# Kernel optimization log

Hardware: AMD Instinct MI355X
Metric: run time of the kernel (lower is better)

The kernel has to match this reference:

```python
import jax, jax.numpy as jnp
import numpy as np

T, B, U = 256, 4, 64
E_ENC, E_DEC, J, V = 1024, 640, 640, 4096
LN_EPS = 1e-5


def layer_norm(x, gamma, beta):
    mu = jnp.mean(x, axis=-1, keepdims=True)
    var = jnp.mean(jnp.square(x - mu), axis=-1, keepdims=True)
    return (x - mu) * jax.lax.rsqrt(var + LN_EPS) * gamma + beta


def setup_inputs() -> dict:
    key = jax.random.key(0)
    ks = jax.random.split(key, 8)
    inp = {
        "encoder_out": jax.random.normal(ks[0], (T, B, E_ENC), dtype=jnp.float32),
        "decoder_out": jax.random.normal(ks[1], (U, B, E_DEC), dtype=jnp.float32),
        # proj_encoder
        "W_enc": jax.random.normal(ks[2], (J, E_ENC), dtype=jnp.float32) * (E_ENC ** -0.5),
        "b_enc": jnp.zeros((J,), dtype=jnp.float32),
        "g_enc": jnp.ones((J,), dtype=jnp.float32),
        "be_enc": jnp.zeros((J,), dtype=jnp.float32),
        # proj_decoder
        "W_dec": jax.random.normal(ks[3], (J, E_DEC), dtype=jnp.float32) * (E_DEC ** -0.5),
        "b_dec": jnp.zeros((J,), dtype=jnp.float32),
        "g_dec": jnp.ones((J,), dtype=jnp.float32),
        "be_dec": jnp.zeros((J,), dtype=jnp.float32),
        # fc_out (init.normal_ with std = joint_dim**-0.5)
        "W_out": jax.random.normal(ks[4], (V, J), dtype=jnp.float32) * (J ** -0.5),
        "b_out": jnp.zeros((V,), dtype=jnp.float32),
    }
    return inp


def reference(encoder_out, decoder_out, W_enc, b_enc, g_enc, be_enc,
              W_dec, b_dec, g_dec, be_dec, W_out, b_out):
    # encoder_out: [T, B, E_enc] -> project+LN -> transpose -> [B, T, J]
    enc = layer_norm(jnp.einsum('tbe,je->tbj', encoder_out, W_enc) + b_enc,
                     g_enc, be_enc).transpose(1, 0, 2)
    # decoder_out: [U, B, E_dec] -> [B, U, J]
    dec = layer_norm(jnp.einsum('ube,je->ubj', decoder_out, W_dec) + b_dec,
                     g_dec, be_dec).transpose(1, 0, 2)
    # broadcast outer-sum over T x U, then ReLU: [B, T, U, J]
    joint = jax.nn.relu(enc[:, :, None, :] + dec[:, None, :, :])
    # vocab projection: [B, T, U, V]
    return jnp.einsum('btuj,vj->btuv', joint, W_out) + b_out
```

## Files before the change

### kernel.cpp

```cpp
#include <hip/hip_runtime.h>
#include <stdint.h>

#define T_    256
#define B_    4
#define U_    64
#define EENC  1024
#define EDEC  640
#define J_    640
#define V_    4096

typedef unsigned short u16;
typedef unsigned int   u32;
typedef __bf16 bf16x8 __attribute__((ext_vector_type(8)));
typedef short  s16x8  __attribute__((ext_vector_type(8)));
typedef float  f32x4  __attribute__((ext_vector_type(4)));

__device__ __forceinline__ u16 f2bf(float f) {
    u32 u = __builtin_bit_cast(u32, f);
    u = (u + 0x7FFFu + ((u >> 16) & 1u)) >> 16;
    return (u16)u;
}
__device__ __forceinline__ float bf2f(u16 b) {
    return __builtin_bit_cast(float, (u32)b << 16);
}

__global__ __launch_bounds__(256) void cvt_bf16(const float* __restrict__ src,
                                                u16* __restrict__ dst, int n4) {
    int i = blockIdx.x * 256 + threadIdx.x;
    if (i < n4) {
        float4 v = reinterpret_cast<const float4*>(src)[i];
        ushort4 o;
        o.x = f2bf(v.x); o.y = f2bf(v.y); o.z = f2bf(v.z); o.w = f2bf(v.w);
        reinterpret_cast<ushort4*>(dst)[i] = o;
    }
}

__global__ __launch_bounds__(256) void ln_kernel(const float* __restrict__ proj,
                                                 const float* __restrict__ bias,
                                                 const float* __restrict__ gamma,
                                                 const float* __restrict__ beta,
                                                 u16* __restrict__ out,
                                                 int BDIM, int OUTER) {
    int pr = blockIdx.x;
    int b = pr % BDIM, outer = pr / BDIM;
    const float* row = proj + (size_t)pr * J_;
    int tid = threadIdx.x;

    float x0 = row[tid] + bias[tid];
    float x1 = row[tid + 256] + bias[tid + 256];
    float x2 = 0.f;
    bool has3 = (tid < J_ - 512);
    if (has3) x2 = row[tid + 512] + bias[tid + 512];

    float s1 = x0 + x1 + x2;
    float s2 = x0 * x0 + x1 * x1 + x2 * x2;
    for (int off = 32; off; off >>= 1) {
        s1 += __shfl_down(s1, off, 64);
        s2 += __shfl_down(s2, off, 64);
    }
    __shared__ float ws1[4], ws2[4];
    int w = tid >> 6, lane = tid & 63;
    if (lane == 0) { ws1[w] = s1; ws2[w] = s2; }
    __syncthreads();
    float S1 = ws1[0] + ws1[1] + ws1[2] + ws1[3];
    float S2 = ws2[0] + ws2[1] + ws2[2] + ws2[3];
    float mu = S1 * (1.f / J_);
    float var = S2 * (1.f / J_) - mu * mu;
    float inv = 1.0f / sqrtf(var + 1e-5f);

    size_t orow = ((size_t)b * OUTER + outer) * J_;
    out[orow + tid]       = f2bf((x0 - mu) * inv * gamma[tid]       + beta[tid]);
    out[orow + tid + 256] = f2bf((x1 - mu) * inv * gamma[tid + 256] + beta[tid + 256]);
    if (has3)
        out[orow + tid + 512] = f2bf((x2 - mu) * inv * gamma[tid + 512] + beta[tid + 512]);
}

__global__ __launch_bounds__(256) void joint_mat(const u16* __restrict__ encln,
                                                 const u16* __restrict__ decln,
                                                 u16* __restrict__ joint) {
    int g = blockIdx.x * 256 + threadIdx.x;
    int row = g / (J_ / 8);
    int jc = g - row * (J_ / 8);
    int b = row >> 14;
    int t = (row >> 6) & (T_ - 1);
    int u = row & (U_ - 1);
    s16x8 e = *reinterpret_cast<const s16x8*>(encln + ((size_t)(b * T_ + t)) * J_ + jc * 8);
    s16x8 d = *reinterpret_cast<const s16x8*>(decln + ((size_t)(b * U_ + u)) * J_ + jc * 8);
    s16x8 o;
#pragma unroll
    for (int k = 0; k < 8; ++k) {
        float v = bf2f((u16)e[k]) + bf2f((u16)d[k]);
        o[k] = (short)f2bf(fmaxf(v, 0.f));
    }
    *reinterpret_cast<s16x8*>(joint + (size_t)row * J_ + jc * 8) = o;
}

__global__ __launch_bounds__(256) void gemm_bt(const u16* __restrict__ A,
                                               const u16* __restrict__ Bt,
                                               float* __restrict__ C,
                                               const float* __restrict__ bias,
                                               int K, int ldc) {
    __shared__ u16 As[128 * 64];
    __shared__ u16 Bs[128 * 64];
    const int tid = threadIdx.x;
    const int w = tid >> 6, lane = tid & 63;
    const int wr = w >> 1, wc = w & 1;
    const size_t m0 = (size_t)blockIdx.y * 128;
    const size_t n0 = (size_t)blockIdx.x * 128;

    f32x4 acc[4][4] = {};

    const int l3 = lane >> 3;
    const int c8 = (lane & 7) * 8;
    const int nkt = K >> 6;

    for (int kt = 0; kt < nkt; ++kt) {
        if (kt) __syncthreads();
        const int k0 = kt << 6;
#pragma unroll
        for (int i = 0; i < 4; ++i) {
            const int c = w * 4 + i;
            const int r = c * 8 + l3;
            const u16* ga = A  + (m0 + r) * (size_t)K + k0 + c8;
            const u16* gb = Bt + (n0 + r) * (size_t)K + k0 + c8;
            __builtin_amdgcn_global_load_lds(
                (const __attribute__((address_space(1))) void*)ga,
                (__attribute__((address_space(3))) void*)(As + c * 512), 16, 0, 0);
            __builtin_amdgcn_global_load_lds(
                (const __attribute__((address_space(1))) void*)gb,
                (__attribute__((address_space(3))) void*)(Bs + c * 512), 16, 0, 0);
        }
        __syncthreads();

#pragma unroll
        for (int kk = 0; kk < 2; ++kk) {
            bf16x8 af[4], bfr[4];
#pragma unroll
            for (int i = 0; i < 4; ++i) {
                int ra = wr * 64 + i * 16 + (lane & 15);
                af[i] = *reinterpret_cast<const bf16x8*>(As + ra * 64 + kk * 32 + (lane >> 4) * 8);
                int rb = wc * 64 + i * 16 + (lane & 15);
                bfr[i] = *reinterpret_cast<const bf16x8*>(Bs + rb * 64 + kk * 32 + (lane >> 4) * 8);
            }
#pragma unroll
            for (int i = 0; i < 4; ++i)
#pragma unroll
                for (int j = 0; j < 4; ++j)
                    acc[i][j] = __builtin_amdgcn_mfma_f32_16x16x32_bf16(af[i], bfr[j], acc[i][j], 0, 0, 0);
        }
    }

    const int r4 = (lane >> 4) * 4;
    const int cl = lane & 15;
#pragma unroll
    for (int i = 0; i < 4; ++i) {
#pragma unroll
        for (int j = 0; j < 4; ++j) {
            size_t grow = m0 + wr * 64 + i * 16 + r4;
            size_t gcol = n0 + wc * 64 + j * 16 + cl;
            float bv = bias ? bias[gcol] : 0.f;
#pragma unroll
            for (int r = 0; r < 4; ++r)
                C[(grow + r) * (size_t)ldc + gcol] = acc[i][j][r] + bv;
        }
    }
}

#define BK   64
#define BIGK 640
#define BIGN 4096
#define NT_  (BIGK / BK)

__global__ __launch_bounds__(512, 2) void gemm_big(const u16* __restrict__ A,
                                                   const u16* __restrict__ Bt,
                                                   float* __restrict__ C,
                                                   const float* __restrict__ bias) {
    __shared__ u16 lds[2][2][256 * BK];

    const int tid = threadIdx.x;
    const int w = tid >> 6, lane = tid & 63;
    const int wr = w >> 2, wc = w & 3;
    const int fr = lane & 15, fq = lane >> 4;

    const int lin = blockIdx.x;
    const int xcd = lin & 7;
    const int idx = lin >> 3;
    const size_t m0 = (size_t)(idx >> 1) * 256;
    const size_t n0 = (size_t)(xcd * 2 + (idx & 1)) * 256;

    const int srow = lane >> 3;
    const int scol = ((lane & 7) * 16) ^ (srow << 4);
    const u16* agbase = A  + (m0 + w * 8 + srow) * (size_t)BIGK + (scol >> 1);
    const u16* bgbase = Bt + (n0 + w * 8 + srow) * (size_t)BIGK + (scol >> 1);
    const int ldst = (w * 8) * BK;

    f32x4 acc[8][4] = {};

#define STAGE_A(buf, c, k0)                                                        \
    __builtin_amdgcn_global_load_lds(                                              \
        (const __attribute__((address_space(1))) void*)(agbase + (size_t)(c) * 64 * BIGK + (k0)), \
        (__attribute__((address_space(3))) void*)(&lds[buf][0][(c) * 64 * BK + ldst]), 16, 0, 0)
#define STAGE_B(buf, c, k0)                                                        \
    __builtin_amdgcn_global_load_lds(                                              \
        (const __attribute__((address_space(1))) void*)(bgbase + (size_t)(c) * 64 * BIGK + (k0)), \
        (__attribute__((address_space(3))) void*)(&lds[buf][1][(c) * 64 * BK + ldst]), 16, 0, 0)

#define RD_A(buf, mh, mi, kk)                                                      \
    (*reinterpret_cast<const bf16x8*>(&lds[buf][0][                                \
        (wr * 128 + (mh) * 64 + (mi) * 16 + fr) * BK +                             \
        ((((kk) * 64 + fq * 16) ^ ((fr & 7) << 4)) >> 1)]))
#define RD_B(buf, ni, kk)                                                          \
    (*reinterpret_cast<const bf16x8*>(&lds[buf][1][                                \
        (wc * 64 + (ni) * 16 + fr) * BK +                                          \
        ((((kk) * 64 + fq * 16) ^ ((fr & 7) << 4)) >> 1)]))

#define WAIT2 asm volatile("s_waitcnt vmcnt(2)" ::: "memory")
#define WAIT0 asm volatile("s_waitcnt vmcnt(0)" ::: "memory")
#define LGKM0 asm volatile("s_waitcnt lgkmcnt(0)" ::: "memory")

    STAGE_B(0, 0, 0); STAGE_B(0, 1, 0); STAGE_B(0, 2, 0); STAGE_B(0, 3, 0);
    STAGE_A(0, 0, 0); STAGE_A(0, 2, 0); STAGE_A(0, 1, 0); STAGE_A(0, 3, 0);
    WAIT2;
    __builtin_amdgcn_s_barrier();

    for (int t = 0; t < NT_; ++t) {
        const int cur = t & 1, nxt = cur ^ 1;
        const int kn = (t + 1) << 6;
        const bool pf = (t + 1 < NT_);
        bf16x8 af[4], b0[4], b1[4];

#pragma unroll
        for (int i = 0; i < 4; ++i) af[i] = RD_A(cur, 0, i, 0);
#pragma unroll
        for (int j = 0; j < 4; ++j) b0[j] = RD_B(cur, j, 0);
        if (pf) { STAGE_B(nxt, 0, kn); STAGE_B(nxt, 1, kn); }
        __builtin_amdgcn_s_barrier();
        LGKM0;
        __builtin_amdgcn_s_setprio(1);
#pragma unroll
        for (int i = 0; i < 4; ++i)
#pragma unroll
            for (int j = 0; j < 4; ++j)
                acc[i][j] = __builtin_amdgcn_mfma_f32_16x16x32_bf16(af[i], b0[j], acc[i][j], 0, 0, 0);
        __builtin_amdgcn_s_setprio(0);
        if (pf) WAIT2; else WAIT0;
        __builtin_amdgcn_s_barrier();

#pragma unroll
        for (int i = 0; i < 4; ++i) af[i] = RD_A(cur, 1, i, 0);
        if (pf) { STAGE_B(nxt, 2, kn); STAGE_B(nxt, 3, kn); }
        __builtin_amdgcn_s_barrier();
        LGKM0;
        __builtin_amdgcn_s_setprio(1);
#pragma unroll
        for (int i = 0; i < 4; ++i)
#pragma unroll
            for (int j = 0; j < 4; ++j)
                acc[4 + i][j] = __builtin_amdgcn_mfma_f32_16x16x32_bf16(af[i], b0[j], acc[4 + i][j], 0, 0, 0);
        __builtin_amdgcn_s_setprio(0);
        __builtin_amdgcn_s_barrier();

#pragma unroll
        for (int i = 0; i < 4; ++i) af[i] = RD_A(cur, 0, i, 1);
#pragma unroll
        for (int j = 0; j < 4; ++j) b1[j] = RD_B(cur, j, 1);
        if (pf) { STAGE_A(nxt, 0, kn); STAGE_A(nxt, 2, kn); }
        __builtin_amdgcn_s_barrier();
        LGKM0;
        __builtin_amdgcn_s_setprio(1);
#pragma unroll
        for (int i = 0; i < 4; ++i)
#pragma unroll
            for (int j = 0; j < 4; ++j)
                acc[i][j] = __builtin_amdgcn_mfma_f32_16x16x32_bf16(af[i], b1[j], acc[i][j], 0, 0, 0);
        __builtin_amdgcn_s_setprio(0);
        __builtin_amdgcn_s_barrier();

#pragma unroll
        for (int i = 0; i < 4; ++i) af[i] = RD_A(cur, 1, i, 1);
        if (pf) { STAGE_A(nxt, 1, kn); STAGE_A(nxt, 3, kn); }
        __builtin_amdgcn_s_barrier();
        LGKM0;
        __builtin_amdgcn_s_setprio(1);
#pragma unroll
        for (int i = 0; i < 4; ++i)
#pragma unroll
            for (int j = 0; j < 4; ++j)
                acc[4 + i][j] = __builtin_amdgcn_mfma_f32_16x16x32_bf16(af[i], b1[j], acc[4 + i][j], 0, 0, 0);
        __builtin_amdgcn_s_setprio(0);
        if (pf) WAIT2;
        __builtin_amdgcn_s_barrier();
    }

#undef STAGE_A
#undef STAGE_B
#undef RD_A
#undef RD_B
#undef WAIT2
#undef WAIT0
#undef LGKM0

    const size_t crow0 = m0 + wr * 128 + fq * 4;
    const size_t ccol0 = n0 + wc * 64 + fr;
#pragma unroll
    for (int ni = 0; ni < 4; ++ni) {
        const size_t col = ccol0 + ni * 16;
        const float bv = bias[col];
#pragma unroll
        for (int mi = 0; mi < 8; ++mi) {
            const size_t rbase = crow0 + mi * 16;
#pragma unroll
            for (int r = 0; r < 4; ++r)
                __builtin_nontemporal_store(acc[mi][ni][r] + bv,
                                            &C[(rbase + r) * (size_t)BIGN + col]);
        }
    }
}

static const size_t O_JOINT = 0;
static const size_t O_WOUT  = 83886080;
static const size_t O_ENCLN = 89128960;
static const size_t O_DECLN = 90439680;
static const size_t O_ENCIN = 90767360;
static const size_t O_DECIN = 92864512;
static const size_t O_WENC  = 93192192;
static const size_t O_WDEC  = 94502912;
static const size_t O_EPROJ = 95322112;
static const size_t O_DPROJ = 97943552;
static const size_t WS_NEEDED = 98598912;

extern "C" void kernel_launch(void* const* d_in, const int* in_sizes, int n_in,
                              void* d_out, int out_size, void* d_ws, size_t ws_size,
                              hipStream_t stream) {
    const float* enc   = (const float*)d_in[0];
    const float* dec   = (const float*)d_in[1];
    const float* Wenc  = (const float*)d_in[2];
    const float* benc  = (const float*)d_in[3];
    const float* genc  = (const float*)d_in[4];
    const float* beenc = (const float*)d_in[5];
    const float* Wdec  = (const float*)d_in[6];
    const float* bdec  = (const float*)d_in[7];
    const float* gdec  = (const float*)d_in[8];
    const float* bedec = (const float*)d_in[9];
    const float* Wout  = (const float*)d_in[10];
    const float* bout  = (const float*)d_in[11];
    float* out = (float*)d_out;

    if (ws_size < WS_NEEDED) return;

    char* ws = (char*)d_ws;
    u16* joint  = (u16*)(ws + O_JOINT);
    u16* wout_b = (u16*)(ws + O_WOUT);
    u16* encln  = (u16*)(ws + O_ENCLN);
    u16* decln  = (u16*)(ws + O_DECLN);
    u16* encin  = (u16*)(ws + O_ENCIN);
    u16* decin  = (u16*)(ws + O_DECIN);
    u16* wenc_b = (u16*)(ws + O_WENC);
    u16* wdec_b = (u16*)(ws + O_WDEC);
    float* eproj = (float*)(ws + O_EPROJ);
    float* dproj = (float*)(ws + O_DPROJ);

    cvt_bf16<<<1024, 256, 0, stream>>>(enc,  encin,  (T_ * B_ * EENC) / 4);
    cvt_bf16<<<160,  256, 0, stream>>>(dec,  decin,  (U_ * B_ * EDEC) / 4);
    cvt_bf16<<<640,  256, 0, stream>>>(Wenc, wenc_b, (J_ * EENC) / 4);
    cvt_bf16<<<400,  256, 0, stream>>>(Wdec, wdec_b, (J_ * EDEC) / 4);
    cvt_bf16<<<2560, 256, 0, stream>>>(Wout, wout_b, (V_ * J_) / 4);

    gemm_bt<<<dim3(J_ / 128, (T_ * B_) / 128), 256, 0, stream>>>(encin, wenc_b, eproj, nullptr, EENC, J_);
    gemm_bt<<<dim3(J_ / 128, (U_ * B_) / 128), 256, 0, stream>>>(decin, wdec_b, dproj, nullptr, EDEC, J_);

    ln_kernel<<<T_ * B_, 256, 0, stream>>>(eproj, benc, genc, beenc, encln, B_, T_);
    ln_kernel<<<U_ * B_, 256, 0, stream>>>(dproj, bdec, gdec, bedec, decln, B_, U_);

    joint_mat<<<(B_ * T_ * U_ * (J_ / 8)) / 256, 256, 0, stream>>>(encln, decln, joint);

    gemm_big<<<(B_ * T_ * U_ / 256) * (V_ / 256), 512, 0, stream>>>(joint, wout_b, out, bout);
}
```

Measured before the change: 533.6 us.

## Fuse joint add+ReLU into big GEMM A-tile loading, drop joint buffer

Removes the separate joint_mat kernel and its large bf16 joint intermediate. The big GEMM now builds its A tile on the fly: it loads encoder and decoder LN rows into registers, adds them, applies ReLU, packs to bf16 and writes the result into swizzled LDS. This saves an extra write and read of the joint tensor in HBM. In exchange, A staging goes through registers instead of async global_load_lds, and the pipeline waits change to full vmcnt(0), which may expose more load latency.

Result: slower. 617.6 us (+15.7%).

```diff
diff --git a/kernel.cpp b/kernel.cpp
--- a/kernel.cpp
+++ b/kernel.cpp
@@ -22,6 +22,24 @@
 }
 __device__ __forceinline__ float bf2f(u16 b) {
     return __builtin_bit_cast(float, (u32)b << 16);
+}
+
+__device__ __forceinline__ u32 joint2(u32 e, u32 d) {
+    float elo = __builtin_bit_cast(float, e << 16);
+    float ehi = __builtin_bit_cast(float, e & 0xFFFF0000u);
+    float dlo = __builtin_bit_cast(float, d << 16);
+    float dhi = __builtin_bit_cast(float, d & 0xFFFF0000u);
+    float slo = fmaxf(elo + dlo, 0.f);
+    float shi = fmaxf(ehi + dhi, 0.f);
+    u32 r;
+    asm("v_cvt_pk_bf16_f32 %0, %1, %2" : "=v"(r) : "v"(slo), "v"(shi));
+    return r;
+}
+__device__ __forceinline__ uint4 joint4(uint4 e, uint4 d) {
+    uint4 j;
+    j.x = joint2(e.x, d.x); j.y = joint2(e.y, d.y);
+    j.z = joint2(e.z, d.z); j.w = joint2(e.w, d.w);
+    return j;
 }
 
 __global__ __launch_bounds__(256) void cvt_bf16(const float* __restrict__ src,
@@ -73,26 +91,6 @@
     out[orow + tid + 256] = f2bf((x1 - mu) * inv * gamma[tid + 256] + beta[tid + 256]);
     if (has3)
         out[orow + tid + 512] = f2bf((x2 - mu) * inv * gamma[tid + 512] + beta[tid + 512]);
-}
-
-__global__ __launch_bounds__(256) void joint_mat(const u16* __restrict__ encln,
-                                                 const u16* __restrict__ decln,
-                                                 u16* __restrict__ joint) {
-    int g = blockIdx.x * 256 + threadIdx.x;
-    int row = g / (J_ / 8);
-    int jc = g - row * (J_ / 8);
-    int b = row >> 14;
-    int t = (row >> 6) & (T_ - 1);
-    int u = row & (U_ - 1);
-    s16x8 e = *reinterpret_cast<const s16x8*>(encln + ((size_t)(b * T_ + t)) * J_ + jc * 8);
-    s16x8 d = *reinterpret_cast<const s16x8*>(decln + ((size_t)(b * U_ + u)) * J_ + jc * 8);
-    s16x8 o;
-#pragma unroll
-    for (int k = 0; k < 8; ++k) {
-        float v = bf2f((u16)e[k]) + bf2f((u16)d[k]);
-        o[k] = (short)f2bf(fmaxf(v, 0.f));
-    }
-    *reinterpret_cast<s16x8*>(joint + (size_t)row * J_ + jc * 8) = o;
 }
 
 __global__ __launch_bounds__(256) void gemm_bt(const u16* __restrict__ A,
@@ -171,7 +169,8 @@
 #define BIGN 4096
 #define NT_  (BIGK / BK)
 
-__global__ __launch_bounds__(512, 2) void gemm_big(const u16* __restrict__ A,
+__global__ __launch_bounds__(512, 2) void gemm_big(const u16* __restrict__ encln,
+                                                   const u16* __restrict__ decln,
                                                    const u16* __restrict__ Bt,
                                                    float* __restrict__ C,
                                                    const float* __restrict__ bias) {
@@ -185,25 +184,50 @@
     const int lin = blockIdx.x;
     const int xcd = lin & 7;
     const int idx = lin >> 3;
-    const size_t m0 = (size_t)(idx >> 1) * 256;
+    const int mt  = idx >> 1;
+    const size_t m0 = (size_t)mt * 256;
     const size_t n0 = (size_t)(xcd * 2 + (idx & 1)) * 256;
+
+    const int b  = mt >> 6;
+    const int t0 = (mt & 63) << 2;
+
+    const int r  = tid >> 1;
+    const int h  = tid & 1;
+    const int tq = r >> 6;
+    const int uu = r & 63;
+    const int xr = (r & 7) << 4;
+    const u16* encrow = encln + (size_t)(b * T_ + t0 + tq) * J_ + 32 * h;
+    const u16* decrow = decln + (size_t)(b * U_ + uu) * J_ + 32 * h;
+    const int aw0 = r * BK + ((( 0 + 64 * h) ^ xr) >> 1);
+    const int aw1 = r * BK + (((16 + 64 * h) ^ xr) >> 1);
+    const int aw2 = r * BK + (((32 + 64 * h) ^ xr) >> 1);
+    const int aw3 = r * BK + (((48 + 64 * h) ^ xr) >> 1);
 
     const int srow = lane >> 3;
     const int scol = ((lane & 7) * 16) ^ (srow << 4);
-    const u16* agbase = A  + (m0 + w * 8 + srow) * (size_t)BIGK + (scol >> 1);
     const u16* bgbase = Bt + (n0 + w * 8 + srow) * (size_t)BIGK + (scol >> 1);
     const int ldst = (w * 8) * BK;
 
     f32x4 acc[8][4] = {};
 
-#define STAGE_A(buf, c, k0)                                                        \
-    __builtin_amdgcn_global_load_lds(                                              \
-        (const __attribute__((address_space(1))) void*)(agbase + (size_t)(c) * 64 * BIGK + (k0)), \
-        (__attribute__((address_space(3))) void*)(&lds[buf][0][(c) * 64 * BK + ldst]), 16, 0, 0)
 #define STAGE_B(buf, c, k0)                                                        \
     __builtin_amdgcn_global_load_lds(                                              \
         (const __attribute__((address_space(1))) void*)(bgbase + (size_t)(c) * 64 * BIGK + (k0)), \
         (__attribute__((address_space(3))) void*)(&lds[buf][1][(c) * 64 * BK + ldst]), 16, 0, 0)
+
+#define A_LOAD(kt)                                                                 \
+    { const u16* ep = encrow + (size_t)(kt) * BK;                                  \
+      const u16* dp = decrow + (size_t)(kt) * BK;                                  \
+      ev0 = *(const uint4*)(ep);      dv0 = *(const uint4*)(dp);                   \
+      ev1 = *(const uint4*)(ep + 8);  dv1 = *(const uint4*)(dp + 8);               \
+      ev2 = *(const uint4*)(ep + 16); dv2 = *(const uint4*)(dp + 16);              \
+      ev3 = *(const uint4*)(ep + 24); dv3 = *(const uint4*)(dp + 24); }
+
+#define A_WRITE(buf)                                                               \
+    { *(uint4*)(&lds[buf][0][aw0]) = joint4(ev0, dv0);                             \
+      *(uint4*)(&lds[buf][0][aw1]) = joint4(ev1, dv1);                             \
+      *(uint4*)(&lds[buf][0][aw2]) = joint4(ev2, dv2);                             \
+      *(uint4*)(&lds[buf][0][aw3]) = joint4(ev3, dv3); }
 
 #define RD_A(buf, mh, mi, kk)                                                      \
     (*reinterpret_cast<const bf16x8*>(&lds[buf][0][                                \
@@ -214,20 +238,25 @@
         (wc * 64 + (ni) * 16 + fr) * BK +                                          \
         ((((kk) * 64 + fq * 16) ^ ((fr & 7) << 4)) >> 1)]))
 
-#define WAIT2 asm volatile("s_waitcnt vmcnt(2)" ::: "memory")
-#define WAIT0 asm volatile("s_waitcnt vmcnt(0)" ::: "memory")
+#define VM0   asm volatile("s_waitcnt vmcnt(0)" ::: "memory")
 #define LGKM0 asm volatile("s_waitcnt lgkmcnt(0)" ::: "memory")
 
-    STAGE_B(0, 0, 0); STAGE_B(0, 1, 0); STAGE_B(0, 2, 0); STAGE_B(0, 3, 0);
-    STAGE_A(0, 0, 0); STAGE_A(0, 2, 0); STAGE_A(0, 1, 0); STAGE_A(0, 3, 0);
-    WAIT2;
-    __builtin_amdgcn_s_barrier();
+    {
+        uint4 ev0, ev1, ev2, ev3, dv0, dv1, dv2, dv3;
+        STAGE_B(0, 0, 0); STAGE_B(0, 1, 0); STAGE_B(0, 2, 0); STAGE_B(0, 3, 0);
+        A_LOAD(0);
+        A_WRITE(0);
+        VM0;
+        LGKM0;
+        __builtin_amdgcn_s_barrier();
+    }
 
     for (int t = 0; t < NT_; ++t) {
         const int cur = t & 1, nxt = cur ^ 1;
         const int kn = (t + 1) << 6;
         const bool pf = (t + 1 < NT_);
         bf16x8 af[4], b0[4], b1[4];
+        uint4 ev0, ev1, ev2, ev3, dv0, dv1, dv2, dv3;
 
 #pragma unroll
         for (int i = 0; i < 4; ++i) af[i] = RD_A(cur, 0, i, 0);
@@ -243,7 +272,6 @@
             for (int j = 0; j < 4; ++j)
                 acc[i][j] = __builtin_amdgcn_mfma_f32_16x16x32_bf16(af[i], b0[j], acc[i][j], 0, 0, 0);
         __builtin_amdgcn_s_setprio(0);
-        if (pf) WAIT2; else WAIT0;
         __builtin_amdgcn_s_barrier();
 
 #pragma unroll
@@ -264,7 +292,7 @@
         for (int i = 0; i < 4; ++i) af[i] = RD_A(cur, 0, i, 1);
 #pragma unroll
         for (int j = 0; j < 4; ++j) b1[j] = RD_B(cur, j, 1);
-        if (pf) { STAGE_A(nxt, 0, kn); STAGE_A(nxt, 2, kn); }
+        if (pf) A_LOAD(t + 1);
         __builtin_amdgcn_s_barrier();
         LGKM0;
         __builtin_amdgcn_s_setprio(1);
@@ -278,7 +306,8 @@
 
 #pragma unroll
         for (int i = 0; i < 4; ++i) af[i] = RD_A(cur, 1, i, 1);
-        if (pf) { STAGE_A(nxt, 1, kn); STAGE_A(nxt, 3, kn); }
+        if (pf) A_WRITE(nxt);
+        VM0;
         __builtin_amdgcn_s_barrier();
         LGKM0;
         __builtin_amdgcn_s_setprio(1);
@@ -288,16 +317,15 @@
             for (int j = 0; j < 4; ++j)
                 acc[4 + i][j] = __builtin_amdgcn_mfma_f32_16x16x32_bf16(af[i], b1[j], acc[4 + i][j], 0, 0, 0);
         __builtin_amdgcn_s_setprio(0);
-        if (pf) WAIT2;
-        __builtin_amdgcn_s_barrier();
-    }
-
-#undef STAGE_A
+        __builtin_amdgcn_s_barrier();
+    }
+
 #undef STAGE_B
+#undef A_LOAD
+#undef A_WRITE
 #undef RD_A
 #undef RD_B
-#undef WAIT2
-#undef WAIT0
+#undef VM0
 #undef LGKM0
 
     const size_t crow0 = m0 + wr * 128 + fq * 4;
@@ -310,24 +338,23 @@
         for (int mi = 0; mi < 8; ++mi) {
             const size_t rbase = crow0 + mi * 16;
 #pragma unroll
-            for (int r = 0; r < 4; ++r)
-                __builtin_nontemporal_store(acc[mi][ni][r] + bv,
-                                            &C[(rbase + r) * (size_t)BIGN + col]);
+            for (int rr = 0; rr < 4; ++rr)
+                __builtin_nontemporal_store(acc[mi][ni][rr] + bv,
+                                            &C[(rbase + rr) * (size_t)BIGN + col]);
         }
     }
 }
 
-static const size_t O_JOINT = 0;
-static const size_t O_WOUT  = 83886080;
-static const size_t O_ENCLN = 89128960;
-static const size_t O_DECLN = 90439680;
-static const size_t O_ENCIN = 90767360;
-static const size_t O_DECIN = 92864512;
-static const size_t O_WENC  = 93192192;
-static const size_t O_WDEC  = 94502912;
-static const size_t O_EPROJ = 95322112;
-static const size_t O_DPROJ = 97943552;
-static const size_t WS_NEEDED = 98598912;
+static const size_t O_WOUT  = 0;
+static const size_t O_ENCLN = 5242880;
+static const size_t O_DECLN = 6553600;
+static const size_t O_ENCIN = 6881280;
+static const size_t O_DECIN = 8978432;
+static const size_t O_WENC  = 9306112;
+static const size_t O_WDEC  = 10616832;
+static const size_t O_EPROJ = 11436032;
+static const size_t O_DPROJ = 14057472;
+static const size_t WS_NEEDED = 14712832;
 
 extern "C" void kernel_launch(void* const* d_in, const int* in_sizes, int n_in,
                               void* d_out, int out_size, void* d_ws, size_t ws_size,
@@ -349,7 +376,6 @@
     if (ws_size < WS_NEEDED) return;
 
     char* ws = (char*)d_ws;
-    u16* joint  = (u16*)(ws + O_JOINT);
     u16* wout_b = (u16*)(ws + O_WOUT);
     u16* encln  = (u16*)(ws + O_ENCLN);
     u16* decln  = (u16*)(ws + O_DECLN);
@@ -372,7 +398,5 @@
     ln_kernel<<<T_ * B_, 256, 0, stream>>>(eproj, benc, genc, beenc, encln, B_, T_);
     ln_kernel<<<U_ * B_, 256, 0, stream>>>(dproj, bdec, gdec, bedec, decln, B_, U_);
 
-    joint_mat<<<(B_ * T_ * U_ * (J_ / 8)) / 256, 256, 0, stream>>>(encln, decln, joint);
-
-    gemm_big<<<(B_ * T_ * U_ / 256) * (V_ / 256), 512, 0, stream>>>(joint, wout_b, out, bout);
-}
+    gemm_big<<<(B_ * T_ * U_ / 256) * (V_ / 256), 512, 0, stream>>>(encln, decln, wout_b, out, bout);
+}
```
